# Kernel tuning notes

Hardware: AMD Instinct MI355X
Metric: run time of the kernel (lower is better)

The kernel has to match this reference:

```python
import jax, jax.numpy as jnp
import numpy as np

# Static config
B, C, H, W = 1, 4, 64, 64
DIM, NH = 512, 16
HD = DIM // NH
SCALE = HD ** -0.5
WC, WH, WW = 2, 8, 8            # 3D window size
N = WC * WH * WW                # tokens per window = 128
SC, SH, SW = 1, 4, 4            # shift = window // 2
NWC, NWH, NWW = C // WC, H // WH, W // WW
NWIN = NWC * NWH * NWW          # windows per sample
HID = 4 * DIM
NBLK = 2                        # [no-shift, shift] pair


def _rel_idx():
    coords = np.stack(np.meshgrid(np.arange(WC), np.arange(WH), np.arange(WW), indexing='ij')).reshape(3, -1)
    rel = coords[:, :, None] - coords[:, None, :]
    rel[0] += WC - 1; rel[1] += WH - 1; rel[2] += WW - 1
    idx = rel[0] * (2 * WH - 1) * (2 * WW - 1) + rel[1] * (2 * WW - 1) + rel[2]
    return jnp.asarray(idx)  # [N, N] into 675-entry table

REL_IDX = _rel_idx()


def _shift_mask():
    img = np.zeros((C, H, W), np.int32)
    cnt = 0
    for cs in (slice(0, -WC), slice(-WC, -SC), slice(-SC, None)):
        for hs in (slice(0, -WH), slice(-WH, -SH), slice(-SH, None)):
            for ws in (slice(0, -WW), slice(-WW, -SW), slice(-SW, None)):
                img[cs, hs, ws] = cnt; cnt += 1
    img = img.reshape(NWC, WC, NWH, WH, NWW, WW).transpose(0, 2, 4, 1, 3, 5).reshape(NWIN, N)
    diff = img[:, :, None] != img[:, None, :]
    return jnp.asarray(np.where(diff, -100.0, 0.0).astype(np.float32))  # [NWIN, N, N]

MASK = _shift_mask()


def _win_part(x):  # [B,C,H,W,D] -> [B*NWIN, N, D]
    x = x.reshape(B, NWC, WC, NWH, WH, NWW, WW, DIM)
    return x.transpose(0, 1, 3, 5, 2, 4, 6, 7).reshape(B * NWIN, N, DIM)


def _win_rev(x):  # [B*NWIN, N, D] -> [B,C,H,W,D]
    x = x.reshape(B, NWC, NWH, NWW, WC, WH, WW, DIM)
    return x.transpose(0, 1, 4, 2, 5, 3, 6, 7).reshape(B, C, H, W, DIM)


def _ln(x, g, b):
    m = x.mean(-1, keepdims=True)
    v = ((x - m) ** 2).mean(-1, keepdims=True)
    return (x - m) / jnp.sqrt(v + 1e-5) * g + b


def _forward(x, ln1_g, ln1_b, qkv_w, qkv_b, bias_tab, proj_w, proj_b,
             ln2_g, ln2_b, fc1_w, fc1_b, fc2_w, fc2_b):
    for i in range(NBLK):
        shifted = (i % 2 == 1)
        shortcut = x
        h = _ln(x, ln1_g[i], ln1_b[i]).reshape(B, C, H, W, DIM)
        if shifted:
            h = jnp.roll(h, (-SC, -SH, -SW), axis=(1, 2, 3))
        xw = _win_part(h)  # [B*NWIN, N, DIM]
        qkv = (xw @ qkv_w[i] + qkv_b[i]).reshape(-1, N, 3, NH, HD).transpose(2, 0, 3, 1, 4)
        q, k, v = qkv[0] * SCALE, qkv[1], qkv[2]       # [B*NWIN, NH, N, HD]
        bias = bias_tab[i][REL_IDX].transpose(2, 0, 1)  # [NH, N, N]
        attn = jnp.einsum('whnd,whmd->whnm', q, k) + bias[None]
        if shifted:
            attn = (attn.reshape(B, NWIN, NH, N, N) + MASK[None, :, None]).reshape(-1, NH, N, N)
        attn = jax.nn.softmax(attn, axis=-1)
        out = jnp.einsum('whnm,whmd->wnhd', attn, v).reshape(-1, N, DIM)
        out = out @ proj_w[i] + proj_b[i]
        h = _win_rev(out)
        if shifted:
            h = jnp.roll(h, (SC, SH, SW), axis=(1, 2, 3))
        x = shortcut + h.reshape(B, C * H * W, DIM)
        h2 = _ln(x, ln2_g[i], ln2_b[i])
        h2 = jax.nn.gelu(h2 @ fc1_w[i] + fc1_b[i], approximate=False) @ fc2_w[i] + fc2_b[i]
        x = x + h2
    return x


def setup_inputs() -> dict:
    key = jax.random.key(0)
    ks = jax.random.split(key, 8)
    s = 0.02
    return {
        'x': jax.random.normal(ks[0], (B, C * H * W, DIM), jnp.float32),
        'ln1_g': jnp.ones((NBLK, DIM), jnp.float32),
        'ln1_b': jnp.zeros((NBLK, DIM), jnp.float32),
        'qkv_w': jax.random.normal(ks[1], (NBLK, DIM, 3 * DIM), jnp.float32) * s,
        'qkv_b': jnp.zeros((NBLK, 3 * DIM), jnp.float32),
        'bias_tab': jax.random.normal(ks[2], (NBLK, (2 * WC - 1) * (2 * WH - 1) * (2 * WW - 1), NH), jnp.float32) * s,
        'proj_w': jax.random.normal(ks[3], (NBLK, DIM, DIM), jnp.float32) * s,
        'proj_b': jnp.zeros((NBLK, DIM), jnp.float32),
        'ln2_g': jnp.ones((NBLK, DIM), jnp.float32),
        'ln2_b': jnp.zeros((NBLK, DIM), jnp.float32),
        'fc1_w': jax.random.normal(ks[4], (NBLK, DIM, HID), jnp.float32) * s,
        'fc1_b': jnp.zeros((NBLK, HID), jnp.float32),
        'fc2_w': jax.random.normal(ks[5], (NBLK, HID, DIM), jnp.float32) * s,
        'fc2_b': jnp.zeros((NBLK, DIM), jnp.float32),
    }


def reference(x, ln1_g, ln1_b, qkv_w, qkv_b, bias_tab, proj_w, proj_b,
              ln2_g, ln2_b, fc1_w, fc1_b, fc2_w, fc2_b):
    return _forward(x, ln1_g, ln1_b, qkv_w, qkv_b, bias_tab, proj_w, proj_b,
                    ln2_g, ln2_b, fc1_w, fc1_b, fc2_w, fc2_b)
```

## Files before the change

### kernel.cpp

```cpp
#include <hip/hip_runtime.h>
#include <stdint.h>

#define DIM 512
#define NHD 16
#define HD 32
#define NTOK 16384

typedef unsigned short u16;
typedef __attribute__((ext_vector_type(8))) short short8;
typedef __attribute__((ext_vector_type(4))) float f32x4;

__device__ __forceinline__ float bf2f(u16 u){ union{unsigned i; float f;} c; c.i=(unsigned)u<<16; return c.f; }
__device__ __forceinline__ float bflo(unsigned u){ union{unsigned i; float f;} c; c.i=u<<16; return c.f; }
__device__ __forceinline__ float bfhi(unsigned u){ union{unsigned i; float f;} c; c.i=u&0xffff0000u; return c.f; }
__device__ __forceinline__ u16 f2bf(float f){ union{float f; unsigned i;} c; c.f=f; unsigned r=(c.i + 0x7fffu + ((c.i>>16)&1u))>>16; return (u16)r; }

__device__ __forceinline__ int win_to_tok(int r, int shifted){
  int win = r >> 7, n = r & 127;
  int a = win >> 6, b = (win >> 3) & 7, c = win & 7;
  int ic = n >> 6, ih = (n >> 3) & 7, iw = n & 7;
  int gc = a*2 + ic, gh = b*8 + ih, gw = c*8 + iw;
  if (shifted){ gc = (gc + 1) & 3; gh = (gh + 4) & 63; gw = (gw + 4) & 63; }
  return (gc << 12) + (gh << 6) + gw;
}

__device__ __forceinline__ void gload16(const void* g, void* l){
  __builtin_amdgcn_global_load_lds(
    (const __attribute__((address_space(1))) unsigned int*)(unsigned long long)g,
    (__attribute__((address_space(3))) unsigned int*)(unsigned int)(unsigned long long)l,
    16, 0, 0);
}

__global__ __launch_bounds__(256)
void transpose_kernel(const float* __restrict__ W, u16* __restrict__ Wt, int K, int N)
{
  __shared__ float t[32][33];
  int n0 = blockIdx.x*32, k0 = blockIdx.y*32;
  int tx = threadIdx.x & 31, ty = threadIdx.x >> 5;
  #pragma unroll
  for (int i=0;i<4;i++) t[ty + i*8][tx] = W[(size_t)(k0 + ty + i*8)*N + n0 + tx];
  __syncthreads();
  #pragma unroll
  for (int i=0;i<4;i++) Wt[(size_t)(n0 + ty + i*8)*K + k0 + tx] = f2bf(t[tx][ty + i*8]);
}

__global__ __launch_bounds__(256)
void ln_kernel(const float* __restrict__ x, const float* __restrict__ g,
               const float* __restrict__ b, u16* __restrict__ out, int mode)
{
  int wave = threadIdx.x >> 6, lane = threadIdx.x & 63;
  int r = blockIdx.x * 4 + wave;
  int src = (mode < 0) ? r : win_to_tok(r, mode);
  const float4* xr = (const float4*)(x + (size_t)src * DIM);
  float4 v0 = xr[lane*2], v1 = xr[lane*2+1];
  float s  = v0.x+v0.y+v0.z+v0.w+v1.x+v1.y+v1.z+v1.w;
  float sq = v0.x*v0.x+v0.y*v0.y+v0.z*v0.z+v0.w*v0.w
           + v1.x*v1.x+v1.y*v1.y+v1.z*v1.z+v1.w*v1.w;
  #pragma unroll
  for (int o=32;o;o>>=1){ s += __shfl_xor(s,o); sq += __shfl_xor(sq,o); }
  float mean = s*(1.f/DIM);
  float var  = sq*(1.f/DIM) - mean*mean;
  float rstd = rsqrtf(var + 1e-5f);
  int c0 = lane*8;
  const float4* g4 = (const float4*)(g + c0);
  const float4* b4 = (const float4*)(b + c0);
  float4 ga = g4[0], gb = g4[1], ba = b4[0], bb = b4[1];
  float xv[8] = {v0.x,v0.y,v0.z,v0.w,v1.x,v1.y,v1.z,v1.w};
  float gg[8] = {ga.x,ga.y,ga.z,ga.w,gb.x,gb.y,gb.z,gb.w};
  float bv[8] = {ba.x,ba.y,ba.z,ba.w,bb.x,bb.y,bb.z,bb.w};
  union{u16 us[8]; uint4 u;} p;
  #pragma unroll
  for (int j=0;j<8;j++) p.us[j] = f2bf((xv[j]-mean)*rstd*gg[j] + bv[j]);
  ((uint4*)(out + (size_t)r*DIM))[lane] = p.u;
}

template<int EPI>
__global__ __launch_bounds__(256)
void gemm_kernel(const u16* __restrict__ X, const u16* __restrict__ Wt,
                 const float* __restrict__ bias, u16* __restrict__ obf,
                 float* __restrict__ xres, int M, int N, int K, int shifted)
{
  __shared__ u16 As[128*64];
  __shared__ u16 Bs[128*64];
  int tid = threadIdx.x, wave = tid>>6, lane = tid&63;
  int nwg = gridDim.x * gridDim.y;
  int bid = blockIdx.y * gridDim.x + blockIdx.x;
  int wg  = (bid & 7) * (nwg >> 3) + (bid >> 3);
  int n0 = (wg % gridDim.x) * 128;
  int m0 = (wg / gridDim.x) * 128;
  int wm = (wave>>1)*64, wn = (wave&1)*64;
  f32x4 acc[4][4] = {};
  int srow = tid>>3;
  int soff = (((tid&7) ^ ((tid>>3)&7)))*8;

  for (int k0=0; k0<K; k0+=64){
    __syncthreads();
    #pragma unroll
    for (int i=0;i<4;i++)
      gload16(X + (size_t)(m0 + i*32 + srow)*K + k0 + soff, (void*)(As + (i*256 + wave*64)*8));
    #pragma unroll
    for (int i=0;i<4;i++)
      gload16(Wt + (size_t)(n0 + i*32 + srow)*K + k0 + soff, (void*)(Bs + (i*256 + wave*64)*8));
    __syncthreads();
    #pragma unroll
    for (int kk=0; kk<64; kk+=32){
      short8 af[4], bfr[4];
      #pragma unroll
      for (int mi=0;mi<4;mi++)
        af[mi] = *(const short8*)(As + (wm + mi*16 + (lane&15))*64 + ((kk + (lane>>4)*8) ^ ((lane&7)<<3)));
      #pragma unroll
      for (int nj=0;nj<4;nj++)
        bfr[nj] = *(const short8*)(Bs + (wn + nj*16 + (lane&15))*64 + ((kk + (lane>>4)*8) ^ ((lane&7)<<3)));
      #pragma unroll
      for (int mi=0;mi<4;mi++)
        #pragma unroll
        for (int nj=0;nj<4;nj++)
          acc[mi][nj] = __builtin_amdgcn_mfma_f32_16x16x32_bf16(af[mi], bfr[nj], acc[mi][nj], 0,0,0);
    }
  }

  int lr = (lane>>4)*4, lc = lane&15;
  #pragma unroll
  for (int mi=0;mi<4;mi++){
    #pragma unroll
    for (int nj=0;nj<4;nj++){
      int col = n0 + wn + nj*16 + lc;
      float bv = bias[col];
      #pragma unroll
      for (int rr=0;rr<4;rr++){
        int row = m0 + wm + mi*16 + lr + rr;
        float v = acc[mi][nj][rr] + bv;
        if (EPI==0){
          obf[(size_t)row*N + col] = f2bf(v);
        } else if (EPI==1){
          int dst = win_to_tok(row, shifted);
          xres[(size_t)dst*DIM + col] += v;
        } else if (EPI==2){
          float t = 0.5f*v*(1.f + erff(v*0.70710678118654752f));
          obf[(size_t)row*N + col] = f2bf(t);
        } else {
          xres[(size_t)row*DIM + col] += v;
        }
      }
    }
  }
}

__global__ __launch_bounds__(256)
void bias_kernel(const float* __restrict__ btab, float* __restrict__ biasM)
{
  int gid = blockIdx.x*256 + threadIdx.x;
  int q = (gid >> 7) & 127, k = gid & 127, h = gid >> 14;
  int ic=q>>6, ih=(q>>3)&7, iw=q&7, jc=k>>6, jh=(k>>3)&7, jw=k&7;
  int idx = (ic-jc+1)*225 + (ih-jh+7)*15 + (iw-jw+7);
  biasM[gid] = btab[idx*16 + h];
}

__global__ __launch_bounds__(256)
void attn_kernel(const u16* __restrict__ qkv, const float* __restrict__ biasM,
                 u16* __restrict__ out, int shifted)
{
  __shared__ u16 Ks[128*32];
  __shared__ u16 VsT[32*128];
  __shared__ u16 Ps[4][32*128];
  __shared__ int rid[128];
  int win = blockIdx.x >> 4, h = blockIdx.x & 15;
  int tid = threadIdx.x, wave = tid>>6, lane = tid&63;
  size_t base = (size_t)win*128*1536 + (size_t)h*32;

  {
    int m = tid>>1, half = tid&1;
    const uint4* ks = (const uint4*)(qkv + base + (size_t)m*1536 + 512 + half*16);
    uint4 k0v = ks[0], k1v = ks[1];
    char* krow = (char*)Ks + m*64;
    int c0 = half*32, sw = (m&3)<<4;
    *(uint4*)(krow + ((c0     ) ^ sw)) = k0v;
    *(uint4*)(krow + ((c0 + 16) ^ sw)) = k1v;
    const uint4* vs = (const uint4*)(qkv + base + (size_t)m*1536 + 1024 + half*16);
    union{u16 us[16]; uint4 u[2];} vv; vv.u[0]=vs[0]; vv.u[1]=vs[1];
    #pragma unroll
    for (int j=0;j<16;j++){
      int d = half*16 + j;
      *(u16*)((char*)VsT + ((d*256 + m*2) ^ ((d&7)<<4))) = vv.us[j];
    }
  }
  if (shifted && tid < 128){
    int a=win>>6, b=(win>>3)&7, c=win&7;
    int gc=a*2+(tid>>6), gh=b*8+((tid>>3)&7), gw=c*8+(tid&7);
    int rc = (gc<2)?0:((gc<3)?1:2);
    int rh = (gh<56)?0:((gh<60)?1:2);
    int rw = (gw<56)?0:((gw<60)?1:2);
    rid[tid] = rc*9 + rh*3 + rw;
  }
  __syncthreads();

  int q0 = wave*32;
  short8 qf[2];
  #pragma unroll
  for (int mi=0;mi<2;mi++){
    int ql = 16*mi + (lane&15);
    qf[mi] = *(const short8*)(qkv + base + (size_t)(q0+ql)*1536 + (lane>>4)*8);
  }
  f32x4 s[2][8] = {};
  #pragma unroll
  for (int nj=0;nj<8;nj++){
    int row = (lane&15) + 16*nj;
    short8 kf = *(const short8*)((char*)Ks + row*64 + ((((lane>>4)<<4)) ^ ((row&3)<<4)));
    #pragma unroll
    for (int mi=0;mi<2;mi++)
      s[mi][nj] = __builtin_amdgcn_mfma_f32_16x16x32_bf16(qf[mi], kf, s[mi][nj], 0,0,0);
  }

  int rk[8];
  if (shifted){
    #pragma unroll
    for (int nj=0;nj<8;nj++) rk[nj] = rid[(lane&15) + 16*nj];
  }
  float invl[2][4];
  char* pbase = (char*)Ps[wave];
  #pragma unroll
  for (int mi=0;mi<2;mi++){
    #pragma unroll
    for (int r=0;r<4;r++){
      int ql = 16*mi + ((lane>>4)<<2) + r;
      int qw = q0 + ql;
      const float* bp = biasM + (((h<<7) + qw)<<7) + (lane&15);
      int rq = shifted ? rid[qw] : 0;
      float sv[8]; float mx = -1e30f;
      #pragma unroll
      for (int nj=0;nj<8;nj++){
        float v = s[mi][nj][r] * 0.17677669529663687f + bp[nj*16];
        if (shifted && rk[nj] != rq) v -= 100.f;
        sv[nj] = v; mx = fmaxf(mx, v);
      }
      #pragma unroll
      for (int o=1;o<16;o<<=1) mx = fmaxf(mx, __shfl_xor(mx, o));
      float sum = 0.f;
      #pragma unroll
      for (int nj=0;nj<8;nj++){ float p = __expf(sv[nj]-mx); sv[nj]=p; sum += p; }
      #pragma unroll
      for (int o=1;o<16;o<<=1) sum += __shfl_xor(sum, o);
      invl[mi][r] = 1.f/sum;
      char* prow = pbase + ql*256;
      int sw = (ql&7)<<4;
      #pragma unroll
      for (int nj=0;nj<8;nj++)
        *(u16*)(prow + ((((lane&15) + (nj<<4))<<1) ^ sw)) = f2bf(sv[nj]);
    }
  }

  f32x4 o2[2][2] = {};
  #pragma unroll
  for (int kk=0;kk<4;kk++){
    int coff = kk*64 + ((lane>>4)<<4);
    short8 pa[2], vb[2];
    #pragma unroll
    for (int mi=0;mi<2;mi++){
      int ql = 16*mi + (lane&15);
      pa[mi] = *(const short8*)(pbase + ql*256 + (coff ^ ((ql&7)<<4)));
    }
    #pragma unroll
    for (int nj=0;nj<2;nj++){
      int d = (lane&15) + 16*nj;
      vb[nj] = *(const short8*)((char*)VsT + d*256 + (coff ^ ((d&7)<<4)));
    }
    #pragma unroll
    for (int mi=0;mi<2;mi++)
      #pragma unroll
      for (int nj=0;nj<2;nj++)
        o2[mi][nj] = __builtin_amdgcn_mfma_f32_16x16x32_bf16(pa[mi], vb[nj], o2[mi][nj], 0,0,0);
  }

  #pragma unroll
  for (int mi=0;mi<2;mi++){
    #pragma unroll
    for (int nj=0;nj<2;nj++){
      #pragma unroll
      for (int r=0;r<4;r++){
        int ql = 16*mi + ((lane>>4)<<2) + r;
        int d  = (lane&15) + (nj<<4);
        out[(size_t)(win*128 + q0 + ql)*DIM + (h<<5) + d] = f2bf(o2[mi][nj][r] * invl[mi][r]);
      }
    }
  }
}

extern "C" void kernel_launch(void* const* d_in, const int* in_sizes, int n_in,
                              void* d_out, int out_size, void* d_ws, size_t ws_size,
                              hipStream_t stream)
{
  const float* x_in   = (const float*)d_in[0];
  const float* ln1_g  = (const float*)d_in[1];
  const float* ln1_b  = (const float*)d_in[2];
  const float* qkv_w  = (const float*)d_in[3];
  const float* qkv_b  = (const float*)d_in[4];
  const float* btab   = (const float*)d_in[5];
  const float* proj_w = (const float*)d_in[6];
  const float* proj_b = (const float*)d_in[7];
  const float* ln2_g  = (const float*)d_in[8];
  const float* ln2_b  = (const float*)d_in[9];
  const float* fc1_w  = (const float*)d_in[10];
  const float* fc1_b  = (const float*)d_in[11];
  const float* fc2_w  = (const float*)d_in[12];
  const float* fc2_b  = (const float*)d_in[13];

  char* ws = (char*)d_ws;
  size_t off = 0;
  auto alloc = [&](size_t bytes)->char*{ char* p = ws + off; off += (bytes + 255) & ~(size_t)255; return p; };
  u16* wT_qkv = (u16*)alloc((size_t)2*512*1536*2);
  u16* wT_proj= (u16*)alloc((size_t)2*512*512*2);
  u16* wT_fc1 = (u16*)alloc((size_t)2*2048*512*2);
  u16* wT_fc2 = (u16*)alloc((size_t)2*512*2048*2);
  u16* bufA   = (u16*)alloc((size_t)16384*2048*2);
  u16* bufQ   = (u16*)alloc((size_t)16384*1536*2);
  u16* bufB   = (u16*)alloc((size_t)16384*512*2);
  float* biasM= (float*)alloc((size_t)16*128*128*4);
  (void)ws_size; (void)in_sizes; (void)n_in; (void)out_size;

  float* x = (float*)d_out;
  hipMemcpyAsync(x, x_in, (size_t)NTOK*DIM*4, hipMemcpyDeviceToDevice, stream);

  for (int i=0;i<2;i++){
    transpose_kernel<<<dim3(1536/32, 512/32), 256, 0, stream>>>(qkv_w + (size_t)i*512*1536, wT_qkv + (size_t)i*512*1536, 512, 1536);
    transpose_kernel<<<dim3( 512/32, 512/32), 256, 0, stream>>>(proj_w + (size_t)i*512*512,  wT_proj + (size_t)i*512*512,  512, 512);
    transpose_kernel<<<dim3(2048/32, 512/32), 256, 0, stream>>>(fc1_w + (size_t)i*512*2048, wT_fc1 + (size_t)i*2048*512, 512, 2048);
    transpose_kernel<<<dim3( 512/32,2048/32), 256, 0, stream>>>(fc2_w + (size_t)i*2048*512, wT_fc2 + (size_t)i*512*2048, 2048, 512);
  }

  for (int i=0;i<2;i++){
    ln_kernel<<<4096, 256, 0, stream>>>(x, ln1_g+i*512, ln1_b+i*512, bufA, i);
    gemm_kernel<0><<<dim3(12,128), 256, 0, stream>>>(bufA, wT_qkv+(size_t)i*512*1536, qkv_b+i*1536, bufQ, nullptr, NTOK,1536,512, 0);
    bias_kernel<<<1024, 256, 0, stream>>>(btab + (size_t)i*675*16, biasM);
    attn_kernel<<<2048, 256, 0, stream>>>(bufQ, biasM, bufB, i);
    gemm_kernel<1><<<dim3(4,128), 256, 0, stream>>>(bufB, wT_proj+(size_t)i*512*512, proj_b+i*512, nullptr, x, NTOK,512,512, i);
    ln_kernel<<<4096, 256, 0, stream>>>(x, ln2_g+i*512, ln2_b+i*512, bufB, -1);
    gemm_kernel<2><<<dim3(16,128), 256, 0, stream>>>(bufB, wT_fc1+(size_t)i*2048*512, fc1_b+i*2048, bufA, nullptr, NTOK,2048,512, 0);
    gemm_kernel<3><<<dim3(4,128), 256, 0, stream>>>(bufA, wT_fc2+(size_t)i*512*2048, fc2_b+i*512, nullptr, x, NTOK,512,2048, 0);
  }
}
```

Baseline: 461.4 us.

## Double-buffer GEMM LDS tiles and stage epilogue through shared memory for coalesced stores

```diff
diff --git a/kernel.cpp b/kernel.cpp
--- a/kernel.cpp
+++ b/kernel.cpp
@@ -80,8 +80,7 @@
                  const float* __restrict__ bias, u16* __restrict__ obf,
                  float* __restrict__ xres, int M, int N, int K, int shifted)
 {
-  __shared__ u16 As[128*64];
-  __shared__ u16 Bs[128*64];
+  __shared__ u16 smem[4][128*64];
   int tid = threadIdx.x, wave = tid>>6, lane = tid&63;
   int nwg = gridDim.x * gridDim.y;
   int bid = blockIdx.y * gridDim.x + blockIdx.x;
@@ -93,55 +92,99 @@
   int srow = tid>>3;
   int soff = (((tid&7) ^ ((tid>>3)&7)))*8;
 
-  for (int k0=0; k0<K; k0+=64){
-    __syncthreads();
+  auto stage = [&](int c, int k0){
     #pragma unroll
     for (int i=0;i<4;i++)
-      gload16(X + (size_t)(m0 + i*32 + srow)*K + k0 + soff, (void*)(As + (i*256 + wave*64)*8));
+      gload16(X + (size_t)(m0 + i*32 + srow)*K + k0 + soff, (void*)(smem[c] + i*2048 + wave*512));
     #pragma unroll
     for (int i=0;i<4;i++)
-      gload16(Wt + (size_t)(n0 + i*32 + srow)*K + k0 + soff, (void*)(Bs + (i*256 + wave*64)*8));
-    __syncthreads();
+      gload16(Wt + (size_t)(n0 + i*32 + srow)*K + k0 + soff, (void*)(smem[2+c] + i*2048 + wave*512));
+  };
+
+  stage(0, 0);
+  __syncthreads();
+  int nkt = K >> 6;
+  for (int kt=0; kt<nkt; ++kt){
+    int c = kt & 1;
+    if (kt+1 < nkt) stage(c^1, (kt+1)<<6);
+    const u16* Ab = smem[c];
+    const u16* Bb = smem[2+c];
     #pragma unroll
     for (int kk=0; kk<64; kk+=32){
       short8 af[4], bfr[4];
+      int cofs = (kk + (lane>>4)*8) ^ ((lane&7)<<3);
       #pragma unroll
       for (int mi=0;mi<4;mi++)
-        af[mi] = *(const short8*)(As + (wm + mi*16 + (lane&15))*64 + ((kk + (lane>>4)*8) ^ ((lane&7)<<3)));
+        af[mi] = *(const short8*)(Ab + (wm + mi*16 + (lane&15))*64 + cofs);
       #pragma unroll
       for (int nj=0;nj<4;nj++)
-        bfr[nj] = *(const short8*)(Bs + (wn + nj*16 + (lane&15))*64 + ((kk + (lane>>4)*8) ^ ((lane&7)<<3)));
+        bfr[nj] = *(const short8*)(Bb + (wn + nj*16 + (lane&15))*64 + cofs);
+      __builtin_amdgcn_s_setprio(1);
       #pragma unroll
       for (int mi=0;mi<4;mi++)
         #pragma unroll
         for (int nj=0;nj<4;nj++)
           acc[mi][nj] = __builtin_amdgcn_mfma_f32_16x16x32_bf16(af[mi], bfr[nj], acc[mi][nj], 0,0,0);
-    }
+      __builtin_amdgcn_s_setprio(0);
+    }
+    __syncthreads();
   }
 
   int lr = (lane>>4)*4, lc = lane&15;
-  #pragma unroll
-  for (int mi=0;mi<4;mi++){
-    #pragma unroll
-    for (int nj=0;nj<4;nj++){
-      int col = n0 + wn + nj*16 + lc;
-      float bv = bias[col];
-      #pragma unroll
-      for (int rr=0;rr<4;rr++){
-        int row = m0 + wm + mi*16 + lr + rr;
-        float v = acc[mi][nj][rr] + bv;
-        if (EPI==0){
-          obf[(size_t)row*N + col] = f2bf(v);
-        } else if (EPI==1){
-          int dst = win_to_tok(row, shifted);
-          xres[(size_t)dst*DIM + col] += v;
-        } else if (EPI==2){
-          float t = 0.5f*v*(1.f + erff(v*0.70710678118654752f));
-          obf[(size_t)row*N + col] = f2bf(t);
-        } else {
-          xres[(size_t)row*DIM + col] += v;
+  if (EPI==0 || EPI==2){
+    u16* et = (u16*)smem;
+    #pragma unroll
+    for (int mi=0;mi<4;mi++){
+      #pragma unroll
+      for (int nj=0;nj<4;nj++){
+        int col = wn + nj*16 + lc;
+        float bv = bias[n0 + col];
+        #pragma unroll
+        for (int rr=0;rr<4;rr++){
+          int row = wm + mi*16 + lr + rr;
+          float v = acc[mi][nj][rr] + bv;
+          if (EPI==2){
+            float u2 = v*(1.5957691216057308f + 0.0713548162726f*v*v);
+            v = v * __builtin_amdgcn_rcpf(1.f + __expf(-u2));
+          }
+          *(u16*)((char*)et + ((row*256 + col*2) ^ (((row>>2)&3)<<5))) = f2bf(v);
         }
       }
+    }
+    __syncthreads();
+    #pragma unroll
+    for (int j=0;j<8;j++){
+      int q = j*256 + tid;
+      int row = q>>4, cc = q&15;
+      uint4 d = *(const uint4*)((char*)et + ((row*256 + cc*16) ^ (((row>>2)&3)<<5)));
+      *(uint4*)(obf + (size_t)(m0+row)*N + n0 + cc*8) = d;
+    }
+  } else {
+    float* et = (float*)smem;
+    #pragma unroll
+    for (int mi=0;mi<4;mi++){
+      #pragma unroll
+      for (int nj=0;nj<4;nj++){
+        int col = wn + nj*16 + lc;
+        float bv = bias[n0 + col];
+        #pragma unroll
+        for (int rr=0;rr<4;rr++){
+          int row = wm + mi*16 + lr + rr;
+          *(float*)((char*)et + ((row*512 + col*4) ^ (((row>>2)&1)<<6))) = acc[mi][nj][rr] + bv;
+        }
+      }
+    }
+    __syncthreads();
+    #pragma unroll
+    for (int j=0;j<16;j++){
+      int q = j*256 + tid;
+      int row = q>>5, cc = q&31;
+      float4 d = *(const float4*)((char*)et + ((row*512 + cc*16) ^ (((row>>2)&1)<<6)));
+      int grow = (EPI==1) ? win_to_tok(m0+row, shifted) : (m0+row);
+      float4* p = (float4*)(xres + (size_t)grow*DIM + n0 + cc*4);
+      float4 o = *p;
+      o.x += d.x; o.y += d.y; o.z += d.z; o.w += d.w;
+      *p = o;
     }
   }
 }
```

Result: faster. 435.8 us (-5.5%).
